# Performance work log

Hardware: AMD Instinct MI355X
Metric: run time of the kernel (lower is better)

## Reference

```python
import jax, jax.numpy as jnp
import numpy as np

B, T, C = 2, 2048, 1024
N_HEAD = 16
D_HEAD = C // N_HEAD


def setup_inputs() -> dict:
    key = jax.random.key(0)
    ks = jax.random.split(key, 5)
    x = jax.random.normal(ks[0], (B, T, C), dtype=jnp.float32)
    W_attn = jax.random.normal(ks[1], (C, 3 * C), dtype=jnp.float32) * (1.0 / np.sqrt(C))
    b_attn = jax.random.normal(ks[2], (3 * C,), dtype=jnp.float32) * 0.02
    W_proj = jax.random.normal(ks[3], (C, C), dtype=jnp.float32) * (1.0 / np.sqrt(C))
    b_proj = jax.random.normal(ks[4], (C,), dtype=jnp.float32) * 0.02
    return {"x": x, "W_attn": W_attn, "b_attn": b_attn, "W_proj": W_proj, "b_proj": b_proj}


def reference(x, W_attn, b_attn, W_proj, b_proj):
    b, t, c = x.shape
    nh, dh = N_HEAD, c // N_HEAD
    # qkv projection: (B, T, 3C) -> (B, T, 3, nh, dh) -> (B, nh, 3, T, dh)
    a = (x @ W_attn + b_attn).reshape(b, t, 3, nh, dh).transpose(0, 3, 2, 1, 4)
    Q, K, V = a[:, :, 0], a[:, :, 1], a[:, :, 2]  # each (B, nh, T, dh)
    # naive full attention: no causal mask, no pre-softmax scaling (as in source)
    scores = jnp.einsum('bhqd,bhkd->bhqk', Q, K)  # (B, nh, T, T) -- 512 MB
    att = jax.nn.softmax(scores, axis=-1)
    y = jnp.einsum('bhqk,bhkd->bhqd', att, V) / jnp.sqrt(jnp.asarray(dh, x.dtype))
    y = y.transpose(0, 2, 1, 3).reshape(b, t, c)  # (B, T, C)
    return y @ W_proj + b_proj
```

## Files before the change

kernel.cpp:

```cpp
#include <hip/hip_runtime.h>

typedef _Float16 f16;
typedef f16  f16x8 __attribute__((ext_vector_type(8)));
typedef f16  f16x4 __attribute__((ext_vector_type(4)));
typedef float f32x4 __attribute__((ext_vector_type(4)));
typedef int  i32x4 __attribute__((ext_vector_type(4)));

#define MFMA16(a,b,c) __builtin_amdgcn_mfma_f32_16x16x32_f16((a),(b),(c),0,0,0)
#define EXP2(x) __builtin_amdgcn_exp2f(x)
#define LOG2E 1.44269504089f

static constexpr int Tq   = 2048;
static constexpr int Cdim = 1024;

__device__ static inline void gload_lds16(const f16* gsrc, f16* ldst)
{
    __builtin_amdgcn_global_load_lds(
        (const __attribute__((address_space(1))) void*)gsrc,
        (__attribute__((address_space(3))) void*)ldst, 16, 0, 0);
}

__global__ __launch_bounds__(256) void k_cvt_x(const float* __restrict__ x, f16* __restrict__ xh)
{
    int i = blockIdx.x * 256 + threadIdx.x;
    f32x4 v = ((const f32x4*)x)[i];
    f16x4 o; o[0] = (f16)v[0]; o[1] = (f16)v[1]; o[2] = (f16)v[2]; o[3] = (f16)v[3];
    ((f16x4*)xh)[i] = o;
}

__global__ __launch_bounds__(256) void k_trans(const float* __restrict__ W, f16* __restrict__ WT,
                                               int K, int N)
{
    __shared__ float t[64][65];
    int n0 = blockIdx.x * 64, k0 = blockIdx.y * 64;
    int tid = threadIdx.x;
    int lr = tid >> 6, lc = tid & 63;
    #pragma unroll 4
    for (int i = 0; i < 16; i++) {
        int kl = lr * 16 + i;
        t[kl][lc] = W[(size_t)(k0 + kl) * N + n0 + lc];
    }
    __syncthreads();
    #pragma unroll 4
    for (int i = 0; i < 16; i++) {
        int nl = lr * 16 + i;
        WT[(size_t)(n0 + nl) * K + k0 + lc] = (f16)t[lc][nl];
    }
}

template<int EPI>
__global__ __launch_bounds__(256) void k_gemm(
    const f16* __restrict__ A, const f16* __restrict__ BT, const float* __restrict__ bias,
    float* __restrict__ Cf, f16* __restrict__ Qc, f16* __restrict__ Kc, f16* __restrict__ Vt,
    int N, int K)
{
    __shared__ __align__(16) f16 As[128][64];
    __shared__ __align__(16) f16 Bs[128][64];
    const int tid = threadIdx.x;
    const int lane = tid & 63, wv = tid >> 6;
    const int l16 = lane & 15, lhi = lane >> 4;
    const int wr = wv >> 1, wc = wv & 1;
    const int bm = blockIdx.y * 128, bn = blockIdx.x * 128;

    const int srow = lane >> 3;
    const int sch  = (lane & 7) ^ (srow & 7);

    f32x4 acc[4][4] = {};

    for (int kt = 0; kt < K; kt += 64) {
        #pragma unroll
        for (int i = 0; i < 4; i++) {
            int blk = wv * 4 + i;
            int row = blk * 8 + srow;
            gload_lds16(A  + (size_t)(bm + row) * K + kt + sch * 8, &As[blk * 8][0]);
            gload_lds16(BT + (size_t)(bn + row) * K + kt + sch * 8, &Bs[blk * 8][0]);
        }
        __syncthreads();
        #pragma unroll
        for (int kk = 0; kk < 2; kk++) {
            f16x8 af[4], bfr[4];
            #pragma unroll
            for (int i = 0; i < 4; i++) {
                int ra = wr * 64 + i * 16 + l16;
                af[i]  = *(const f16x8*)&As[ra][((kk * 4 + lhi) ^ (ra & 7)) * 8];
                int rb = wc * 64 + i * 16 + l16;
                bfr[i] = *(const f16x8*)&Bs[rb][((kk * 4 + lhi) ^ (rb & 7)) * 8];
            }
            #pragma unroll
            for (int i = 0; i < 4; i++)
                #pragma unroll
                for (int j = 0; j < 4; j++)
                    acc[i][j] = MFMA16(af[i], bfr[j], acc[i][j]);
        }
        __syncthreads();
    }

    #pragma unroll
    for (int i = 0; i < 4; i++) {
        int row0 = bm + wr * 64 + i * 16 + lhi * 4;
        #pragma unroll
        for (int j = 0; j < 4; j++) {
            int col = bn + wc * 64 + j * 16 + l16;
            float bv = bias[col];
            if (EPI == 0) {
                #pragma unroll
                for (int r = 0; r < 4; r++)
                    Cf[(size_t)(row0 + r) * N + col] = acc[i][j][r] + bv;
            } else {
                int b_ = row0 >> 11;
                int t0 = row0 & 2047;
                int s  = col >> 10;
                int h  = (col >> 6) & 15;
                int d  = col & 63;
                int bh = b_ * 16 + h;
                if (s < 2) {
                    f16* dst = (s == 0 ? Qc : Kc);
                    #pragma unroll
                    for (int r = 0; r < 4; r++)
                        dst[((size_t)bh * Tq + t0 + r) * 64 + d] = (f16)(acc[i][j][r] + bv);
                } else {
                    f16x4 p;
                    #pragma unroll
                    for (int r = 0; r < 4; r++) p[r] = (f16)(acc[i][j][r] + bv);
                    *(f16x4*)&Vt[((size_t)bh * 64 + d) * Tq + t0] = p;
                }
            }
        }
    }
}

__global__ __launch_bounds__(256) void k_attn(
    const f16* __restrict__ Qc, const f16* __restrict__ Kc, const f16* __restrict__ Vt,
    f16* __restrict__ Yc)
{
    __shared__ __align__(16) f16 Ks[64][64];
    __shared__ __align__(16) f16 Vs[64][64];

    const int tid = threadIdx.x;
    const int lane = tid & 63, wv = tid >> 6;
    const int l16 = lane & 15, lhi = lane >> 4;
    const int bh = blockIdx.y;
    const int q0 = blockIdx.x * 64;

    const f16* Qh = Qc + (size_t)bh * Tq * 64;
    const f16* Kh = Kc + (size_t)bh * Tq * 64;
    const f16* Vh = Vt + (size_t)bh * 64 * Tq;

    const int row0 = tid >> 3, ch0 = tid & 7;
    const int rp0  = (((row0 >> 2) & 1) << 4) | (((row0 >> 4) & 1) << 3)
                   | (((row0 >> 3) & 1) << 2) | (row0 & 3);
    const int pchK = ch0 ^ (rp0 & 7);
    const int pchV = ch0 ^ (row0 & 7);

    f16x8 qf[2];
    {
        int qrow = q0 + wv * 16 + l16;
        #pragma unroll
        for (int kk = 0; kk < 2; kk++)
            qf[kk] = *(const f16x8*)(Qh + (size_t)qrow * 64 + kk * 32 + lhi * 8);
    }

    f32x4 o[4] = {};
    float m2 = -3e38f, l = 0.0f;

    f16x8 kr0, kr1, vr0, vr1;
    kr0 = *(const f16x8*)(Kh + (size_t)row0 * 64 + ch0 * 8);
    kr1 = *(const f16x8*)(Kh + (size_t)(row0 + 32) * 64 + ch0 * 8);
    vr0 = *(const f16x8*)(Vh + (size_t)row0 * Tq + ch0 * 8);
    vr1 = *(const f16x8*)(Vh + (size_t)(row0 + 32) * Tq + ch0 * 8);

    for (int t = 0; t < 32; t++) {
        __syncthreads();
        *(f16x8*)&Ks[rp0][pchK * 8]       = kr0;
        *(f16x8*)&Ks[rp0 + 32][pchK * 8]  = kr1;
        *(f16x8*)&Vs[row0][pchV * 8]      = vr0;
        *(f16x8*)&Vs[row0 + 32][pchV * 8] = vr1;
        __syncthreads();
        if (t < 31) {
            int kt2 = (t + 1) * 64;
            kr0 = *(const f16x8*)(Kh + (size_t)(kt2 + row0) * 64 + ch0 * 8);
            kr1 = *(const f16x8*)(Kh + (size_t)(kt2 + row0 + 32) * 64 + ch0 * 8);
            vr0 = *(const f16x8*)(Vh + (size_t)row0 * Tq + kt2 + ch0 * 8);
            vr1 = *(const f16x8*)(Vh + (size_t)(row0 + 32) * Tq + kt2 + ch0 * 8);
        }

        f32x4 s[4];
        #pragma unroll
        for (int ck = 0; ck < 4; ck++) {
            f32x4 acc = {};
            #pragma unroll
            for (int kk = 0; kk < 2; kk++) {
                f16x8 kf = *(const f16x8*)&Ks[ck * 16 + l16][((kk * 4 + lhi) ^ (l16 & 7)) * 8];
                acc = MFMA16(kf, qf[kk], acc);
            }
            s[ck] = acc;
        }

        float tm = fmaxf(
            fmaxf(fmaxf(fmaxf(s[0][0], s[0][1]), fmaxf(s[0][2], s[0][3])),
                  fmaxf(fmaxf(s[1][0], s[1][1]), fmaxf(s[1][2], s[1][3]))),
            fmaxf(fmaxf(fmaxf(s[2][0], s[2][1]), fmaxf(s[2][2], s[2][3])),
                  fmaxf(fmaxf(s[3][0], s[3][1]), fmaxf(s[3][2], s[3][3]))));
        tm = fmaxf(tm, __shfl_xor(tm, 16));
        tm = fmaxf(tm, __shfl_xor(tm, 32));

        if (!__all(tm - m2 <= 8.0f)) {
            float mn = fmaxf(m2, tm);
            float sc = EXP2((m2 - mn) * LOG2E);
            m2 = mn; l *= sc;
            #pragma unroll
            for (int ct = 0; ct < 4; ct++)
                #pragma unroll
                for (int r = 0; r < 4; r++)
                    o[ct][r] *= sc;
        }

        float nm2 = -m2 * LOG2E;
        f32x4 p[4];
        #pragma unroll
        for (int ck = 0; ck < 4; ck++)
            #pragma unroll
            for (int r = 0; r < 4; r++)
                p[ck][r] = EXP2(fmaf(s[ck][r], LOG2E, nm2));

        float su = ((p[0][0] + p[0][1]) + (p[0][2] + p[0][3]))
                 + ((p[1][0] + p[1][1]) + (p[1][2] + p[1][3]))
                 + ((p[2][0] + p[2][1]) + (p[2][2] + p[2][3]))
                 + ((p[3][0] + p[3][1]) + (p[3][2] + p[3][3]));
        su += __shfl_xor(su, 16);
        su += __shfl_xor(su, 32);
        l += su;

        #pragma unroll
        for (int kk2 = 0; kk2 < 2; kk2++) {
            i32x4 w;
            w[0] = __builtin_bit_cast(int, __builtin_amdgcn_cvt_pkrtz(p[2*kk2][0],   p[2*kk2][1]));
            w[1] = __builtin_bit_cast(int, __builtin_amdgcn_cvt_pkrtz(p[2*kk2][2],   p[2*kk2][3]));
            w[2] = __builtin_bit_cast(int, __builtin_amdgcn_cvt_pkrtz(p[2*kk2+1][0], p[2*kk2+1][1]));
            w[3] = __builtin_bit_cast(int, __builtin_amdgcn_cvt_pkrtz(p[2*kk2+1][2], p[2*kk2+1][3]));
            f16x8 pb = __builtin_bit_cast(f16x8, w);
            #pragma unroll
            for (int ct = 0; ct < 4; ct++) {
                f16x8 vf = *(const f16x8*)&Vs[ct * 16 + l16][((kk2 * 4 + lhi) ^ (l16 & 7)) * 8];
                o[ct] = MFMA16(vf, pb, o[ct]);
            }
        }
    }

    const int b_ = bh >> 4, h_ = bh & 15;
    const int q  = q0 + wv * 16 + l16;
    const float inv = 1.0f / (l * 8.0f);
    size_t rb = (size_t)(b_ * Tq + q) * Cdim + h_ * 64;
    #pragma unroll
    for (int ct = 0; ct < 4; ct++) {
        f16x4 y;
        #pragma unroll
        for (int r = 0; r < 4; r++) y[r] = (f16)(o[ct][r] * inv);
        *(f16x4*)&Yc[rb + ct * 16 + lhi * 4] = y;
    }
}

extern "C" void kernel_launch(void* const* d_in, const int* in_sizes, int n_in,
                              void* d_out, int out_size, void* d_ws, size_t ws_size,
                              hipStream_t stream)
{
    (void)in_sizes; (void)n_in; (void)out_size; (void)ws_size;
    const float* x  = (const float*)d_in[0];
    const float* Wa = (const float*)d_in[1];
    const float* ba = (const float*)d_in[2];
    const float* Wp = (const float*)d_in[3];
    const float* bp = (const float*)d_in[4];
    float* out = (float*)d_out;

    char* ws = (char*)d_ws;
    f16* Xh  = (f16*)(ws);
    f16* WaT = (f16*)(ws + (8u  << 20));
    f16* WpT = (f16*)(ws + (14u << 20));
    f16* Qc  = (f16*)(ws + (16u << 20));
    f16* Kc  = (f16*)(ws + (24u << 20));
    f16* Vt  = (f16*)(ws + (32u << 20));
    f16* Yc  = (f16*)(ws + (40u << 20));

    k_cvt_x<<<4096, 256, 0, stream>>>(x, Xh);
    k_trans<<<dim3(48, 16), 256, 0, stream>>>(Wa, WaT, 1024, 3072);
    k_trans<<<dim3(16, 16), 256, 0, stream>>>(Wp, WpT, 1024, 1024);
    k_gemm<1><<<dim3(24, 32), 256, 0, stream>>>(Xh, WaT, ba, nullptr, Qc, Kc, Vt, 3072, 1024);
    k_attn<<<dim3(32, 32), 256, 0, stream>>>(Qc, Kc, Vt, Yc);
    k_gemm<0><<<dim3(8, 32), 256, 0, stream>>>(Yc, WpT, bp, out, nullptr, nullptr, nullptr, 1024, 1024);
}
```

Measured before the change: 213.3 us.

## Double-buffer K/V tiles in LDS and raise wave priority around MFMA

The attention kernel now keeps two LDS buffers for the K and V tiles. The next tile is written into the idle buffer after the current tile's compute, so each iteration needs one barrier instead of two. s_setprio is raised around the QK and PV MFMA blocks so waves issuing matrix work get scheduling priority over waves doing softmax. LDS use doubles to 32KB per block, which could limit how many blocks fit on a CU.

```diff
diff --git a/kernel.cpp b/kernel.cpp
--- a/kernel.cpp
+++ b/kernel.cpp
@@ -133,8 +133,8 @@
     const f16* __restrict__ Qc, const f16* __restrict__ Kc, const f16* __restrict__ Vt,
     f16* __restrict__ Yc)
 {
-    __shared__ __align__(16) f16 Ks[64][64];
-    __shared__ __align__(16) f16 Vs[64][64];
+    __shared__ __align__(16) f16 Ks[2][64][64];
+    __shared__ __align__(16) f16 Vs[2][64][64];
 
     const int tid = threadIdx.x;
     const int lane = tid & 63, wv = tid >> 6;
@@ -168,14 +168,14 @@
     kr1 = *(const f16x8*)(Kh + (size_t)(row0 + 32) * 64 + ch0 * 8);
     vr0 = *(const f16x8*)(Vh + (size_t)row0 * Tq + ch0 * 8);
     vr1 = *(const f16x8*)(Vh + (size_t)(row0 + 32) * Tq + ch0 * 8);
-
+    *(f16x8*)&Ks[0][rp0][pchK * 8]       = kr0;
+    *(f16x8*)&Ks[0][rp0 + 32][pchK * 8]  = kr1;
+    *(f16x8*)&Vs[0][row0][pchV * 8]      = vr0;
+    *(f16x8*)&Vs[0][row0 + 32][pchV * 8] = vr1;
+    __syncthreads();
+
+    int cur = 0;
     for (int t = 0; t < 32; t++) {
-        __syncthreads();
-        *(f16x8*)&Ks[rp0][pchK * 8]       = kr0;
-        *(f16x8*)&Ks[rp0 + 32][pchK * 8]  = kr1;
-        *(f16x8*)&Vs[row0][pchV * 8]      = vr0;
-        *(f16x8*)&Vs[row0 + 32][pchV * 8] = vr1;
-        __syncthreads();
         if (t < 31) {
             int kt2 = (t + 1) * 64;
             kr0 = *(const f16x8*)(Kh + (size_t)(kt2 + row0) * 64 + ch0 * 8);
@@ -184,17 +184,22 @@
             vr1 = *(const f16x8*)(Vh + (size_t)(row0 + 32) * Tq + kt2 + ch0 * 8);
         }
 
+        const f16 (* __restrict__ Kb)[64] = Ks[cur];
+        const f16 (* __restrict__ Vb)[64] = Vs[cur];
+
         f32x4 s[4];
+        __builtin_amdgcn_s_setprio(1);
         #pragma unroll
         for (int ck = 0; ck < 4; ck++) {
             f32x4 acc = {};
             #pragma unroll
             for (int kk = 0; kk < 2; kk++) {
-                f16x8 kf = *(const f16x8*)&Ks[ck * 16 + l16][((kk * 4 + lhi) ^ (l16 & 7)) * 8];
+                f16x8 kf = *(const f16x8*)&Kb[ck * 16 + l16][((kk * 4 + lhi) ^ (l16 & 7)) * 8];
                 acc = MFMA16(kf, qf[kk], acc);
             }
             s[ck] = acc;
         }
+        __builtin_amdgcn_s_setprio(0);
 
         float tm = fmaxf(
             fmaxf(fmaxf(fmaxf(s[0][0], s[0][1]), fmaxf(s[0][2], s[0][3])),
@@ -231,6 +236,7 @@
         su += __shfl_xor(su, 32);
         l += su;
 
+        __builtin_amdgcn_s_setprio(1);
         #pragma unroll
         for (int kk2 = 0; kk2 < 2; kk2++) {
             i32x4 w;
@@ -241,9 +247,20 @@
             f16x8 pb = __builtin_bit_cast(f16x8, w);
             #pragma unroll
             for (int ct = 0; ct < 4; ct++) {
-                f16x8 vf = *(const f16x8*)&Vs[ct * 16 + l16][((kk2 * 4 + lhi) ^ (l16 & 7)) * 8];
+                f16x8 vf = *(const f16x8*)&Vb[ct * 16 + l16][((kk2 * 4 + lhi) ^ (l16 & 7)) * 8];
                 o[ct] = MFMA16(vf, pb, o[ct]);
             }
+        }
+        __builtin_amdgcn_s_setprio(0);
+
+        if (t < 31) {
+            int nxt = cur ^ 1;
+            *(f16x8*)&Ks[nxt][rp0][pchK * 8]       = kr0;
+            *(f16x8*)&Ks[nxt][rp0 + 32][pchK * 8]  = kr1;
+            *(f16x8*)&Vs[nxt][row0][pchV * 8]      = vr0;
+            *(f16x8*)&Vs[nxt][row0 + 32][pchV * 8] = vr1;
+            __syncthreads();
+            cur = nxt;
         }
     }
 
```

Result: no change. 214.0 us (+0.3%).
